# Kernel optimization log

Hardware: AMD Instinct MI355X
Metric: run time of the kernel (lower is better)

Reference implementation:

```python
import jax, jax.numpy as jnp
import numpy as np

N_NODES = 50000
N_EDGES = 800000
D_IN = 128
D_OUT = 128
ALPHA = 0.5


def setup_inputs() -> dict:
    key = jax.random.key(0)
    k1, k2, k3, k4, k5, k6 = jax.random.split(key, 6)
    x = jax.random.normal(k1, (N_NODES, D_IN), dtype=jnp.float32)
    edge_index = jax.random.randint(k2, (2, N_EDGES), 0, N_NODES, dtype=jnp.int32)
    s = 1.0 / np.sqrt(D_IN)  # torch.nn.Linear default init bound
    W_src = jax.random.uniform(k3, (D_IN, D_OUT), jnp.float32, -s, s)
    b_src = jax.random.uniform(k4, (D_OUT,), jnp.float32, -s, s)
    W_dst = jax.random.uniform(k5, (D_IN, D_OUT), jnp.float32, -s, s)
    b_dst = jax.random.uniform(k6, (D_OUT,), jnp.float32, -s, s)
    return {"x": x, "edge_index": edge_index, "W_src": W_src, "b_src": b_src,
            "W_dst": W_dst, "b_dst": b_dst}


def reference(x, edge_index, W_src, b_src, W_dst, b_dst):
    row, col = edge_index[0], edge_index[1]
    ones = jnp.ones((row.shape[0],), dtype=x.dtype)
    # out-degree = row sums of A; in-degree = column sums of A
    out_deg = jax.ops.segment_sum(ones, row, num_segments=N_NODES)
    in_deg = jax.ops.segment_sum(ones, col, num_segments=N_NODES)
    d_out = jnp.where(out_deg > 0, out_deg ** -0.5, 0.0)
    d_in = jnp.where(in_deg > 0, in_deg ** -0.5, 0.0)
    # D_out^{-1/2} A D_in^{-1/2}: per-edge weight. For A^T the normalized
    # weight at (col,row) is d_in[col]*d_out[row] == same weight, transposed scatter.
    w = d_out[row] * d_in[col]  # [E]
    msg_fwd = w[:, None] * x[col]  # [E, D_IN]
    agg_fwd = jax.ops.segment_sum(msg_fwd, row, num_segments=N_NODES)  # adj_norm @ x
    msg_bwd = w[:, None] * x[row]
    agg_bwd = jax.ops.segment_sum(msg_bwd, col, num_segments=N_NODES)  # adj_t_norm @ x
    out = ALPHA * (agg_fwd @ W_src + b_src) + (1.0 - ALPHA) * (agg_bwd @ W_dst + b_dst)
    return out
```

## Files before the change

kernel.cpp:

```cpp
#include <hip/hip_runtime.h>
#include <hip/hip_bf16.h>


constexpr int N_NODES = 50000;
constexpr int N_EDGES = 800000;
constexpr int D = 128;
constexpr int CAP = 48;
constexpr int NPBK = 512;
constexpr int NBUK = (N_NODES + NPBK - 1) / NPBK;
constexpr int ECH = 2048;
constexpr int NCH = (N_EDGES + ECH - 1) / ECH;
constexpr int CAPB = 12288;
constexpr int CVTB = 128;

typedef __bf16 bf16x8 __attribute__((ext_vector_type(8)));
typedef float  f32x4  __attribute__((ext_vector_type(4)));

__global__ __launch_bounds__(256) void k_part(const int* __restrict__ row,
                                              const int* __restrict__ col,
                                              int* __restrict__ tail,
                                              unsigned* __restrict__ part,
                                              const float* __restrict__ Wsrc,
                                              const float* __restrict__ Wdst,
                                              __hip_bfloat16* __restrict__ Wpk,
                                              const float* __restrict__ x,
                                              __hip_bfloat16* __restrict__ xb) {
    const int bid = blockIdx.x;
    if (bid >= NCH * 2 + 16) {
        const float4* x4 = (const float4*)x;
        bf16x8* xb8 = (bf16x8*)xb;
        const int stride = CVTB * 256;
        for (int i = (bid - (NCH * 2 + 16)) * 256 + threadIdx.x;
             i < N_NODES * D / 8; i += stride) {
            float4 v0 = x4[2 * i];
            float4 v1 = x4[2 * i + 1];
            union { bf16x8 v; __hip_bfloat16 e[8]; } u;
            u.e[0] = __float2bfloat16(v0.x); u.e[1] = __float2bfloat16(v0.y);
            u.e[2] = __float2bfloat16(v0.z); u.e[3] = __float2bfloat16(v0.w);
            u.e[4] = __float2bfloat16(v1.x); u.e[5] = __float2bfloat16(v1.y);
            u.e[6] = __float2bfloat16(v1.z); u.e[7] = __float2bfloat16(v1.w);
            xb8[i] = u.v;
        }
        return;
    }
    if (bid >= NCH * 2) {
        int tid = (bid - NCH * 2) * 256 + threadIdx.x;
        int f = tid >> 6;
        int lane = tid & 63;
        int dir = f >> 5;
        int ct = (f >> 2) & 7;
        int ks = f & 3;
        const float* W = dir ? Wdst : Wsrc;
        int k0 = ks * 32 + (lane >> 4) * 8;
        int n = ct * 16 + (lane & 15);
        __hip_bfloat16 v[8];
        #pragma unroll
        for (int j = 0; j < 8; ++j) v[j] = __float2bfloat16(W[(k0 + j) * D + n]);
        *(bf16x8*)&Wpk[(size_t)tid * 8] = *(const bf16x8*)v;
        return;
    }
    __shared__ int cnt[NBUK], base[NBUK], pos[NBUK];
    const int dir = bid & 1;
    const int chunk = bid >> 1;
    const int* dst = dir ? col : row;
    const int* src = dir ? row : col;
    for (int i = threadIdx.x; i < NBUK; i += 256) { cnt[i] = 0; pos[i] = 0; }
    __syncthreads();
    const int e0 = chunk * ECH;
    const int e1 = min(e0 + ECH, N_EDGES);
    for (int e = e0 + threadIdx.x; e < e1; e += 256)
        atomicAdd(&cnt[dst[e] >> 9], 1);
    __syncthreads();
    for (int i = threadIdx.x; i < NBUK; i += 256)
        base[i] = (cnt[i] > 0) ? atomicAdd(&tail[dir * NBUK + i], cnt[i]) : 0;
    __syncthreads();
    for (int e = e0 + threadIdx.x; e < e1; e += 256) {
        int d = dst[e], s = src[e];
        int b = d >> 9;
        int p = base[b] + atomicAdd(&pos[b], 1);
        if (p < CAPB)
            part[((size_t)dir * NBUK + b) * CAPB + p] =
                ((unsigned)(d & (NPBK - 1)) << 16) | (unsigned)s;
    }
}

__global__ __launch_bounds__(256) void k_bin(const int* __restrict__ tail,
                                             const unsigned* __restrict__ part,
                                             unsigned short* __restrict__ binF,
                                             unsigned short* __restrict__ binB,
                                             int* __restrict__ cntF,
                                             int* __restrict__ cntB,
                                             float* __restrict__ sc_row,
                                             float* __restrict__ sc_col) {
    __shared__ alignas(16) unsigned short bins[NPBK * CAP];
    __shared__ int cnt[NPBK];
    const int dir = blockIdx.x & 1;
    const int b = blockIdx.x >> 1;
    for (int i = threadIdx.x; i < NPBK; i += 256) cnt[i] = 0;
    __syncthreads();
    const int n = min(tail[dir * NBUK + b], CAPB);
    const unsigned* p = &part[((size_t)dir * NBUK + b) * CAPB];
    for (int i = threadIdx.x; i < n; i += 256) {
        unsigned ent = p[i];
        int dl = ent >> 16;
        int q = atomicAdd(&cnt[dl], 1);
        if (q < CAP) bins[dl * CAP + q] = (unsigned short)(ent & 0xFFFFu);
    }
    __syncthreads();
    unsigned short* gbin = dir ? binB : binF;
    int* gcnt = dir ? cntB : cntF;
    float* sc = dir ? sc_col : sc_row;
    const int node0 = b * NPBK;
    const int nv = min(NPBK, N_NODES - node0);
    const int nq = nv * (CAP * 2 / 16);
    const uint4* bw = (const uint4*)bins;
    uint4* gw = (uint4*)&gbin[(size_t)node0 * CAP];
    for (int i = threadIdx.x; i < nq; i += 256) gw[i] = bw[i];
    for (int i = threadIdx.x; i < nv; i += 256) {
        int c = cnt[i];
        gcnt[node0 + i] = c;
        sc[node0 + i] = (c > 0) ? rsqrtf((float)c) : 0.f;
    }
}

__device__ __forceinline__ float4 bf4_to_f4(uint2 u) {
    union { unsigned i; float f; } a, b, c, d;
    a.i = u.x << 16;
    b.i = u.x & 0xFFFF0000u;
    c.i = u.y << 16;
    d.i = u.y & 0xFFFF0000u;
    return make_float4(a.f, b.f, c.f, d.f);
}

__device__ __forceinline__ uint2 f4_to_bf4(float4 f) {
    union { uint2 u; __hip_bfloat16 e[4]; } r;
    r.e[0] = __float2bfloat16(f.x);
    r.e[1] = __float2bfloat16(f.y);
    r.e[2] = __float2bfloat16(f.z);
    r.e[3] = __float2bfloat16(f.w);
    return r.u;
}

__global__ __launch_bounds__(256) void k_agg(const unsigned short* __restrict__ binF,
                                             const int* __restrict__ cntF,
                                             const unsigned short* __restrict__ binB,
                                             const int* __restrict__ cntB,
                                             const float* __restrict__ sc_row,
                                             const float* __restrict__ sc_col,
                                             const uint2* __restrict__ xb,
                                             __hip_bfloat16* __restrict__ aggF,
                                             __hip_bfloat16* __restrict__ aggB) {
    const int node = blockIdx.x * 4 + (threadIdx.x >> 6);
    const int lane = threadIdx.x & 63;
    const int half = lane >> 5;
    const int l32 = lane & 31;
    const int nF = min(cntF[node], CAP);
    const int nB = min(cntB[node], CAP);

    int entF = (lane < nF) ? (int)binF[(size_t)node * CAP + lane] : 0;
    int entB = (lane < nB) ? (int)binB[(size_t)node * CAP + lane] : 0;
    float sclF = sc_col[entF];
    float sclB = sc_row[entB];

    const int sTailF = __shfl(entF, (nF > 0) ? nF - 1 : 0);
    const int sTailB = __shfl(entB, (nB > 0) ? nB - 1 : 0);
    const float wTailF = __shfl(sclF, (nF > 0) ? nF - 1 : 0);
    const float wTailB = __shfl(sclB, (nB > 0) ? nB - 1 : 0);

    float4 accF = make_float4(0.f, 0.f, 0.f, 0.f);
    {
        const int npair = nF >> 1;
        int i = 0;
        for (; i + 3 < npair; i += 4) {
            int s0 = __shfl(entF, 2 * i + half);
            int s1 = __shfl(entF, 2 * (i + 1) + half);
            int s2 = __shfl(entF, 2 * (i + 2) + half);
            int s3 = __shfl(entF, 2 * (i + 3) + half);
            float w0 = __shfl(sclF, 2 * i + half);
            float w1 = __shfl(sclF, 2 * (i + 1) + half);
            float w2 = __shfl(sclF, 2 * (i + 2) + half);
            float w3 = __shfl(sclF, 2 * (i + 3) + half);
            uint2 v0 = xb[(size_t)s0 * 32 + l32];
            uint2 v1 = xb[(size_t)s1 * 32 + l32];
            uint2 v2 = xb[(size_t)s2 * 32 + l32];
            uint2 v3 = xb[(size_t)s3 * 32 + l32];
            float4 f0 = bf4_to_f4(v0), f1 = bf4_to_f4(v1);
            float4 f2 = bf4_to_f4(v2), f3 = bf4_to_f4(v3);
            accF.x += w0 * f0.x + w1 * f1.x + w2 * f2.x + w3 * f3.x;
            accF.y += w0 * f0.y + w1 * f1.y + w2 * f2.y + w3 * f3.y;
            accF.z += w0 * f0.z + w1 * f1.z + w2 * f2.z + w3 * f3.z;
            accF.w += w0 * f0.w + w1 * f1.w + w2 * f2.w + w3 * f3.w;
        }
        for (; i < npair; ++i) {
            int s = __shfl(entF, 2 * i + half);
            float w = __shfl(sclF, 2 * i + half);
            float4 f = bf4_to_f4(xb[(size_t)s * 32 + l32]);
            accF.x += w * f.x; accF.y += w * f.y;
            accF.z += w * f.z; accF.w += w * f.w;
        }
        if ((nF & 1) && half == 0) {
            float4 f = bf4_to_f4(xb[(size_t)sTailF * 32 + l32]);
            accF.x += wTailF * f.x; accF.y += wTailF * f.y;
            accF.z += wTailF * f.z; accF.w += wTailF * f.w;
        }
    }
    float4 accB = make_float4(0.f, 0.f, 0.f, 0.f);
    {
        const int npair = nB >> 1;
        int i = 0;
        for (; i + 3 < npair; i += 4) {
            int s0 = __shfl(entB, 2 * i + half);
            int s1 = __shfl(entB, 2 * (i + 1) + half);
            int s2 = __shfl(entB, 2 * (i + 2) + half);
            int s3 = __shfl(entB, 2 * (i + 3) + half);
            float w0 = __shfl(sclB, 2 * i + half);
            float w1 = __shfl(sclB, 2 * (i + 1) + half);
            float w2 = __shfl(sclB, 2 * (i + 2) + half);
            float w3 = __shfl(sclB, 2 * (i + 3) + half);
            uint2 v0 = xb[(size_t)s0 * 32 + l32];
            uint2 v1 = xb[(size_t)s1 * 32 + l32];
            uint2 v2 = xb[(size_t)s2 * 32 + l32];
            uint2 v3 = xb[(size_t)s3 * 32 + l32];
            float4 f0 = bf4_to_f4(v0), f1 = bf4_to_f4(v1);
            float4 f2 = bf4_to_f4(v2), f3 = bf4_to_f4(v3);
            accB.x += w0 * f0.x + w1 * f1.x + w2 * f2.x + w3 * f3.x;
            accB.y += w0 * f0.y + w1 * f1.y + w2 * f2.y + w3 * f3.y;
            accB.z += w0 * f0.z + w1 * f1.z + w2 * f2.z + w3 * f3.z;
            accB.w += w0 * f0.w + w1 * f1.w + w2 * f2.w + w3 * f3.w;
        }
        for (; i < npair; ++i) {
            int s = __shfl(entB, 2 * i + half);
            float w = __shfl(sclB, 2 * i + half);
            float4 f = bf4_to_f4(xb[(size_t)s * 32 + l32]);
            accB.x += w * f.x; accB.y += w * f.y;
            accB.z += w * f.z; accB.w += w * f.w;
        }
        if ((nB & 1) && half == 0) {
            float4 f = bf4_to_f4(xb[(size_t)sTailB * 32 + l32]);
            accB.x += wTailB * f.x; accB.y += wTailB * f.y;
            accB.z += wTailB * f.z; accB.w += wTailB * f.w;
        }
    }

    accF.x += __shfl_xor(accF.x, 32);
    accF.y += __shfl_xor(accF.y, 32);
    accF.z += __shfl_xor(accF.z, 32);
    accF.w += __shfl_xor(accF.w, 32);
    accB.x += __shfl_xor(accB.x, 32);
    accB.y += __shfl_xor(accB.y, 32);
    accB.z += __shfl_xor(accB.z, 32);
    accB.w += __shfl_xor(accB.w, 32);

    if (half == 0) {
        float s = 0.5f * sc_row[node];
        ((uint2*)aggF)[(size_t)node * 32 + l32] =
            f4_to_bf4(make_float4(s * accF.x, s * accF.y, s * accF.z, s * accF.w));
    } else {
        float s = 0.5f * sc_col[node];
        ((uint2*)aggB)[(size_t)node * 32 + l32] =
            f4_to_bf4(make_float4(s * accB.x, s * accB.y, s * accB.z, s * accB.w));
    }
}

__global__ __launch_bounds__(256) void k_gemm_out(const __hip_bfloat16* __restrict__ aggF,
                                                  const __hip_bfloat16* __restrict__ aggB,
                                                  const bf16x8* __restrict__ Wpk,
                                                  const float* __restrict__ b_src,
                                                  const float* __restrict__ b_dst,
                                                  float* __restrict__ out) {
    __shared__ bf16x8 Bs[64 * 64];
    for (int i = threadIdx.x; i < 64 * 64; i += 256) Bs[i] = Wpk[i];

    const int wave = threadIdx.x >> 6;
    const int lane = threadIdx.x & 63;
    const int quad = lane >> 4;
    const int m0 = blockIdx.x * 64 + wave * 16;

    const int arow = min(m0 + (lane & 15), N_NODES - 1);
    bf16x8 aF[4], aB[4];
    #pragma unroll
    for (int ks = 0; ks < 4; ++ks) {
        aF[ks] = *(const bf16x8*)&aggF[(size_t)arow * D + ks * 32 + quad * 8];
        aB[ks] = *(const bf16x8*)&aggB[(size_t)arow * D + ks * 32 + quad * 8];
    }

    __syncthreads();

    const int crow = m0 + quad * 4;
    #pragma unroll
    for (int ct = 0; ct < 8; ++ct) {
        f32x4 c = {0.f, 0.f, 0.f, 0.f};
        #pragma unroll
        for (int ks = 0; ks < 4; ++ks)
            c = __builtin_amdgcn_mfma_f32_16x16x32_bf16(aF[ks], Bs[(ct * 4 + ks) * 64 + lane], c, 0, 0, 0);
        #pragma unroll
        for (int ks = 0; ks < 4; ++ks)
            c = __builtin_amdgcn_mfma_f32_16x16x32_bf16(aB[ks], Bs[(32 + ct * 4 + ks) * 64 + lane], c, 0, 0, 0);
        const int colb = ct * 16 + (lane & 15);
        const float bias = 0.5f * (b_src[colb] + b_dst[colb]);
        #pragma unroll
        for (int r = 0; r < 4; ++r) {
            int nd = crow + r;
            if (nd < N_NODES) out[(size_t)nd * D + colb] = c[r] + bias;
        }
    }
}

extern "C" void kernel_launch(void* const* d_in, const int* in_sizes, int n_in,
                              void* d_out, int out_size, void* d_ws, size_t ws_size,
                              hipStream_t stream) {
    const float* x     = (const float*)d_in[0];
    const int*   edges = (const int*)d_in[1];
    const float* W_src = (const float*)d_in[2];
    const float* b_src = (const float*)d_in[3];
    const float* W_dst = (const float*)d_in[4];
    const float* b_dst = (const float*)d_in[5];
    float* out = (float*)d_out;

    const int* row = edges;
    const int* col = edges + N_EDGES;

    __hip_bfloat16* xb     = (__hip_bfloat16*)d_ws;
    __hip_bfloat16* aggF   = xb + (size_t)N_NODES * D;
    __hip_bfloat16* aggB   = aggF + (size_t)N_NODES * D;
    __hip_bfloat16* Wpk    = aggB + (size_t)N_NODES * D;
    float*          sc_row = (float*)(Wpk + 64 * 512);
    float*          sc_col = sc_row + N_NODES;
    int*            cntF   = (int*)(sc_col + N_NODES);
    int*            cntB   = cntF + N_NODES;
    int*            tail   = cntB + N_NODES;
    unsigned short* binF   = (unsigned short*)(tail + 256);
    unsigned short* binB   = binF + (size_t)N_NODES * CAP;
    unsigned*       part   = (unsigned*)aggF;

    (void)hipMemsetAsync(tail, 0, 256 * sizeof(int), stream);

    const int gP = NCH * 2 + 16 + CVTB;
    const int gB = NBUK * 2;
    const int gA = N_NODES / 4;
    const int gM = (N_NODES + 63) / 64;

    k_part<<<gP, 256, 0, stream>>>(row, col, tail, part, W_src, W_dst, Wpk, x, xb);
    k_bin<<<gB, 256, 0, stream>>>(tail, part, binF, binB, cntF, cntB, sc_row, sc_col);
    k_agg<<<gA, 256, 0, stream>>>(binF, cntF, binB, cntB, sc_row, sc_col,
                                  (const uint2*)xb, aggF, aggB);
    k_gemm_out<<<gM, 256, 0, stream>>>(aggF, aggB, (const bf16x8*)Wpk,
                                       b_src, b_dst, out);
}
```

Baseline: 198.4 us.

## Tile aggregation gather by source-node range for cache locality

Rewrites the aggregation kernel so each wave owns a strided set of destination nodes in one direction and sweeps source-id tiles, only gathering edges whose source falls in the current tile. This aims to keep the gathered feature rows resident in cache during each tile pass. In exchange, every tile pass reloads bins and counts, adds ballot/ctz serialization with at most two gathers in flight, and loads per-edge scales individually, reducing memory-level parallelism.

```diff
diff --git a/kernel.cpp b/kernel.cpp
--- a/kernel.cpp
+++ b/kernel.cpp
@@ -12,6 +12,12 @@
 constexpr int NCH = (N_EDGES + ECH - 1) / ECH;
 constexpr int CAPB = 12288;
 constexpr int CVTB = 128;
+
+constexpr int TSH  = 13;
+constexpr int NT   = (N_NODES + (1 << TSH) - 1) >> TSH;
+constexpr int AGGB = 1024;
+constexpr int DWID = AGGB * 4 / 2;
+constexpr int KMAX = (N_NODES + DWID - 1) / DWID;
 
 typedef __bf16 bf16x8 __attribute__((ext_vector_type(8)));
 typedef float  f32x4  __attribute__((ext_vector_type(4)));
@@ -123,142 +129,74 @@
     }
 }
 
-__device__ __forceinline__ float4 bf4_to_f4(uint2 u) {
-    union { unsigned i; float f; } a, b, c, d;
-    a.i = u.x << 16;
-    b.i = u.x & 0xFFFF0000u;
-    c.i = u.y << 16;
-    d.i = u.y & 0xFFFF0000u;
-    return make_float4(a.f, b.f, c.f, d.f);
-}
-
-__device__ __forceinline__ uint2 f4_to_bf4(float4 f) {
-    union { uint2 u; __hip_bfloat16 e[4]; } r;
-    r.e[0] = __float2bfloat16(f.x);
-    r.e[1] = __float2bfloat16(f.y);
-    r.e[2] = __float2bfloat16(f.z);
-    r.e[3] = __float2bfloat16(f.w);
-    return r.u;
-}
-
-__global__ __launch_bounds__(256) void k_agg(const unsigned short* __restrict__ binF,
-                                             const int* __restrict__ cntF,
-                                             const unsigned short* __restrict__ binB,
-                                             const int* __restrict__ cntB,
-                                             const float* __restrict__ sc_row,
-                                             const float* __restrict__ sc_col,
-                                             const uint2* __restrict__ xb,
-                                             __hip_bfloat16* __restrict__ aggF,
-                                             __hip_bfloat16* __restrict__ aggB) {
-    const int node = blockIdx.x * 4 + (threadIdx.x >> 6);
+__global__ __launch_bounds__(256, 4) void k_agg(const unsigned short* __restrict__ binF,
+                                                const int* __restrict__ cntF,
+                                                const unsigned short* __restrict__ binB,
+                                                const int* __restrict__ cntB,
+                                                const float* __restrict__ sc_row,
+                                                const float* __restrict__ sc_col,
+                                                const unsigned* __restrict__ xb32,
+                                                unsigned* __restrict__ aggF32,
+                                                unsigned* __restrict__ aggB32) {
+    const int wid  = blockIdx.x * 4 + (threadIdx.x >> 6);
     const int lane = threadIdx.x & 63;
-    const int half = lane >> 5;
-    const int l32 = lane & 31;
-    const int nF = min(cntF[node], CAP);
-    const int nB = min(cntB[node], CAP);
-
-    int entF = (lane < nF) ? (int)binF[(size_t)node * CAP + lane] : 0;
-    int entB = (lane < nB) ? (int)binB[(size_t)node * CAP + lane] : 0;
-    float sclF = sc_col[entF];
-    float sclB = sc_row[entB];
-
-    const int sTailF = __shfl(entF, (nF > 0) ? nF - 1 : 0);
-    const int sTailB = __shfl(entB, (nB > 0) ? nB - 1 : 0);
-    const float wTailF = __shfl(sclF, (nF > 0) ? nF - 1 : 0);
-    const float wTailB = __shfl(sclB, (nB > 0) ? nB - 1 : 0);
-
-    float4 accF = make_float4(0.f, 0.f, 0.f, 0.f);
-    {
-        const int npair = nF >> 1;
-        int i = 0;
-        for (; i + 3 < npair; i += 4) {
-            int s0 = __shfl(entF, 2 * i + half);
-            int s1 = __shfl(entF, 2 * (i + 1) + half);
-            int s2 = __shfl(entF, 2 * (i + 2) + half);
-            int s3 = __shfl(entF, 2 * (i + 3) + half);
-            float w0 = __shfl(sclF, 2 * i + half);
-            float w1 = __shfl(sclF, 2 * (i + 1) + half);
-            float w2 = __shfl(sclF, 2 * (i + 2) + half);
-            float w3 = __shfl(sclF, 2 * (i + 3) + half);
-            uint2 v0 = xb[(size_t)s0 * 32 + l32];
-            uint2 v1 = xb[(size_t)s1 * 32 + l32];
-            uint2 v2 = xb[(size_t)s2 * 32 + l32];
-            uint2 v3 = xb[(size_t)s3 * 32 + l32];
-            float4 f0 = bf4_to_f4(v0), f1 = bf4_to_f4(v1);
-            float4 f2 = bf4_to_f4(v2), f3 = bf4_to_f4(v3);
-            accF.x += w0 * f0.x + w1 * f1.x + w2 * f2.x + w3 * f3.x;
-            accF.y += w0 * f0.y + w1 * f1.y + w2 * f2.y + w3 * f3.y;
-            accF.z += w0 * f0.z + w1 * f1.z + w2 * f2.z + w3 * f3.z;
-            accF.w += w0 * f0.w + w1 * f1.w + w2 * f2.w + w3 * f3.w;
-        }
-        for (; i < npair; ++i) {
-            int s = __shfl(entF, 2 * i + half);
-            float w = __shfl(sclF, 2 * i + half);
-            float4 f = bf4_to_f4(xb[(size_t)s * 32 + l32]);
-            accF.x += w * f.x; accF.y += w * f.y;
-            accF.z += w * f.z; accF.w += w * f.w;
-        }
-        if ((nF & 1) && half == 0) {
-            float4 f = bf4_to_f4(xb[(size_t)sTailF * 32 + l32]);
-            accF.x += wTailF * f.x; accF.y += wTailF * f.y;
-            accF.z += wTailF * f.z; accF.w += wTailF * f.w;
-        }
-    }
-    float4 accB = make_float4(0.f, 0.f, 0.f, 0.f);
-    {
-        const int npair = nB >> 1;
-        int i = 0;
-        for (; i + 3 < npair; i += 4) {
-            int s0 = __shfl(entB, 2 * i + half);
-            int s1 = __shfl(entB, 2 * (i + 1) + half);
-            int s2 = __shfl(entB, 2 * (i + 2) + half);
-            int s3 = __shfl(entB, 2 * (i + 3) + half);
-            float w0 = __shfl(sclB, 2 * i + half);
-            float w1 = __shfl(sclB, 2 * (i + 1) + half);
-            float w2 = __shfl(sclB, 2 * (i + 2) + half);
-            float w3 = __shfl(sclB, 2 * (i + 3) + half);
-            uint2 v0 = xb[(size_t)s0 * 32 + l32];
-            uint2 v1 = xb[(size_t)s1 * 32 + l32];
-            uint2 v2 = xb[(size_t)s2 * 32 + l32];
-            uint2 v3 = xb[(size_t)s3 * 32 + l32];
-            float4 f0 = bf4_to_f4(v0), f1 = bf4_to_f4(v1);
-            float4 f2 = bf4_to_f4(v2), f3 = bf4_to_f4(v3);
-            accB.x += w0 * f0.x + w1 * f1.x + w2 * f2.x + w3 * f3.x;
-            accB.y += w0 * f0.y + w1 * f1.y + w2 * f2.y + w3 * f3.y;
-            accB.z += w0 * f0.z + w1 * f1.z + w2 * f2.z + w3 * f3.z;
-            accB.w += w0 * f0.w + w1 * f1.w + w2 * f2.w + w3 * f3.w;
-        }
-        for (; i < npair; ++i) {
-            int s = __shfl(entB, 2 * i + half);
-            float w = __shfl(sclB, 2 * i + half);
-            float4 f = bf4_to_f4(xb[(size_t)s * 32 + l32]);
-            accB.x += w * f.x; accB.y += w * f.y;
-            accB.z += w * f.z; accB.w += w * f.w;
-        }
-        if ((nB & 1) && half == 0) {
-            float4 f = bf4_to_f4(xb[(size_t)sTailB * 32 + l32]);
-            accB.x += wTailB * f.x; accB.y += wTailB * f.y;
-            accB.z += wTailB * f.z; accB.w += wTailB * f.w;
-        }
-    }
-
-    accF.x += __shfl_xor(accF.x, 32);
-    accF.y += __shfl_xor(accF.y, 32);
-    accF.z += __shfl_xor(accF.z, 32);
-    accF.w += __shfl_xor(accF.w, 32);
-    accB.x += __shfl_xor(accB.x, 32);
-    accB.y += __shfl_xor(accB.y, 32);
-    accB.z += __shfl_xor(accB.z, 32);
-    accB.w += __shfl_xor(accB.w, 32);
-
-    if (half == 0) {
-        float s = 0.5f * sc_row[node];
-        ((uint2*)aggF)[(size_t)node * 32 + l32] =
-            f4_to_bf4(make_float4(s * accF.x, s * accF.y, s * accF.z, s * accF.w));
-    } else {
-        float s = 0.5f * sc_col[node];
-        ((uint2*)aggB)[(size_t)node * 32 + l32] =
-            f4_to_bf4(make_float4(s * accB.x, s * accB.y, s * accB.z, s * accB.w));
+    const int dir  = wid & 1;
+    const int dwid = wid >> 1;
+
+    const unsigned short* bin = dir ? binB : binF;
+    const int*   cnt  = dir ? cntB : cntF;
+    const float* sc_s = dir ? sc_row : sc_col;
+    const float* sc_d = dir ? sc_col : sc_row;
+    unsigned*    agg  = dir ? aggB32 : aggF32;
+
+    float2 acc[KMAX];
+    #pragma unroll
+    for (int k = 0; k < KMAX; ++k) acc[k] = make_float2(0.f, 0.f);
+
+    for (int t = 0; t < NT; ++t) {
+        #pragma unroll
+        for (int k = 0; k < KMAX; ++k) {
+            const int node = dwid + k * DWID;
+            if (node < N_NODES) {
+                const int n = min(cnt[node], CAP);
+                int ent = (int)bin[(size_t)node * CAP + min(lane, CAP - 1)];
+                ent = (lane < n) ? ent : 0xFFFF;
+                unsigned long long m = __ballot((ent >> TSH) == t);
+                while (m) {
+                    int i0 = __builtin_ctzll(m); m &= m - 1;
+                    int s0 = __shfl(ent, i0);
+                    unsigned v0 = xb32[(size_t)s0 * 64 + lane];
+                    float w0 = sc_s[s0];
+                    int have1 = (m != 0);
+                    int s1 = 0; unsigned v1 = 0; float w1 = 0.f;
+                    if (have1) {
+                        int i1 = __builtin_ctzll(m); m &= m - 1;
+                        s1 = __shfl(ent, i1);
+                        v1 = xb32[(size_t)s1 * 64 + lane];
+                        w1 = sc_s[s1];
+                    }
+                    union { unsigned u; float f; } a, b;
+                    a.u = v0 << 16; b.u = v0 & 0xFFFF0000u;
+                    acc[k].x += w0 * a.f; acc[k].y += w0 * b.f;
+                    if (have1) {
+                        a.u = v1 << 16; b.u = v1 & 0xFFFF0000u;
+                        acc[k].x += w1 * a.f; acc[k].y += w1 * b.f;
+                    }
+                }
+            }
+        }
+    }
+
+    #pragma unroll
+    for (int k = 0; k < KMAX; ++k) {
+        const int node = dwid + k * DWID;
+        if (node < N_NODES) {
+            float s = 0.5f * sc_d[node];
+            union { unsigned u; __hip_bfloat16 e[2]; } r;
+            r.e[0] = __float2bfloat16(s * acc[k].x);
+            r.e[1] = __float2bfloat16(s * acc[k].y);
+            agg[(size_t)node * 64 + lane] = r.u;
+        }
     }
 }
 
@@ -337,13 +275,12 @@
 
     const int gP = NCH * 2 + 16 + CVTB;
     const int gB = NBUK * 2;
-    const int gA = N_NODES / 4;
     const int gM = (N_NODES + 63) / 64;
 
     k_part<<<gP, 256, 0, stream>>>(row, col, tail, part, W_src, W_dst, Wpk, x, xb);
     k_bin<<<gB, 256, 0, stream>>>(tail, part, binF, binB, cntF, cntB, sc_row, sc_col);
-    k_agg<<<gA, 256, 0, stream>>>(binF, cntF, binB, cntB, sc_row, sc_col,
-                                  (const uint2*)xb, aggF, aggB);
+    k_agg<<<AGGB, 256, 0, stream>>>(binF, cntF, binB, cntB, sc_row, sc_col,
+                                    (const unsigned*)xb, (unsigned*)aggF, (unsigned*)aggB);
     k_gemm_out<<<gM, 256, 0, stream>>>(aggF, aggB, (const bf16x8*)Wpk,
                                        b_src, b_dst, out);
 }
```

Result: slower. 364.2 us (+83.6%).

## Fuse all stages into one persistent cooperative kernel with grid syncs

Applied to the files above, without the earlier changes.

Replaces the memset plus four separate kernel launches with a single cooperative persistent kernel. The stages are convert/pack, partition, bin, aggregate and GEMM, separated by grid.sync and run in grid-stride task loops. Bucket size is halved to 256 nodes so the binning shared memory fits alongside higher occupancy. The GEMM now reads packed weights straight from global memory instead of staging them in LDS. The aim is to remove launch gaps and tail effects between stages, at the cost of grid-wide barriers and fewer blocks resident per stage.

```diff
diff --git a/kernel.cpp b/kernel.cpp
--- a/kernel.cpp
+++ b/kernel.cpp
@@ -1,37 +1,68 @@
 #include <hip/hip_runtime.h>
 #include <hip/hip_bf16.h>
+#include <hip/hip_cooperative_groups.h>
+
+namespace cg = cooperative_groups;
 
 
 constexpr int N_NODES = 50000;
 constexpr int N_EDGES = 800000;
 constexpr int D = 128;
 constexpr int CAP = 48;
-constexpr int NPBK = 512;
+constexpr int NPBK = 256;
 constexpr int NBUK = (N_NODES + NPBK - 1) / NPBK;
 constexpr int ECH = 2048;
 constexpr int NCH = (N_EDGES + ECH - 1) / ECH;
-constexpr int CAPB = 12288;
-constexpr int CVTB = 128;
+constexpr int CAPB = 5120;
 
 typedef __bf16 bf16x8 __attribute__((ext_vector_type(8)));
 typedef float  f32x4  __attribute__((ext_vector_type(4)));
 
-__global__ __launch_bounds__(256) void k_part(const int* __restrict__ row,
-                                              const int* __restrict__ col,
-                                              int* __restrict__ tail,
-                                              unsigned* __restrict__ part,
-                                              const float* __restrict__ Wsrc,
-                                              const float* __restrict__ Wdst,
-                                              __hip_bfloat16* __restrict__ Wpk,
-                                              const float* __restrict__ x,
-                                              __hip_bfloat16* __restrict__ xb) {
-    const int bid = blockIdx.x;
-    if (bid >= NCH * 2 + 16) {
-        const float4* x4 = (const float4*)x;
-        bf16x8* xb8 = (bf16x8*)xb;
-        const int stride = CVTB * 256;
-        for (int i = (bid - (NCH * 2 + 16)) * 256 + threadIdx.x;
-             i < N_NODES * D / 8; i += stride) {
+struct Params {
+    const int* row; const int* col;
+    const float* x; const float* Wsrc; const float* Wdst;
+    const float* bsrc; const float* bdst;
+    __hip_bfloat16* xb;
+    __hip_bfloat16* Wpk;
+    int* tail; unsigned* part;
+    unsigned short* binF; unsigned short* binB;
+    int* cntF; int* cntB;
+    float* sc_row; float* sc_col;
+    __hip_bfloat16* aggF; __hip_bfloat16* aggB;
+    float* out;
+};
+
+__global__ __launch_bounds__(256, 4) void k_all(Params P) {
+    cg::grid_group grid = cg::this_grid();
+    const int bid  = blockIdx.x;
+    const int nblk = gridDim.x;
+    const int tid  = threadIdx.x;
+    const int wave = tid >> 6;
+    const int lane = tid & 63;
+
+    __shared__ union {
+        struct { int cnt[NBUK]; int base[NBUK]; int pos[NBUK]; } p1;
+        struct { alignas(16) unsigned short bins[NPBK * CAP]; int cnt[NPBK]; } p2;
+    } sh;
+
+    if (bid == 0)
+        for (int i = tid; i < 2 * NBUK; i += 256) P.tail[i] = 0;
+    if (bid >= 1 && bid <= 16) {
+        int t = (bid - 1) * 256 + tid;
+        int f = t >> 6, l = t & 63;
+        int dir = f >> 5, ct = (f >> 2) & 7, ks = f & 3;
+        const float* W = dir ? P.Wdst : P.Wsrc;
+        int k0 = ks * 32 + (l >> 4) * 8;
+        int n = ct * 16 + (l & 15);
+        __hip_bfloat16 v[8];
+        #pragma unroll
+        for (int j = 0; j < 8; ++j) v[j] = __float2bfloat16(W[(k0 + j) * D + n]);
+        *(bf16x8*)&P.Wpk[(size_t)t * 8] = *(const bf16x8*)v;
+    }
+    {
+        const float4* x4 = (const float4*)P.x;
+        bf16x8* xb8 = (bf16x8*)P.xb;
+        for (int i = bid * 256 + tid; i < N_NODES * D / 8; i += nblk * 256) {
             float4 v0 = x4[2 * i];
             float4 v1 = x4[2 * i + 1];
             union { bf16x8 v; __hip_bfloat16 e[8]; } u;
@@ -41,267 +72,255 @@
             u.e[6] = __float2bfloat16(v1.z); u.e[7] = __float2bfloat16(v1.w);
             xb8[i] = u.v;
         }
-        return;
-    }
-    if (bid >= NCH * 2) {
-        int tid = (bid - NCH * 2) * 256 + threadIdx.x;
-        int f = tid >> 6;
-        int lane = tid & 63;
-        int dir = f >> 5;
-        int ct = (f >> 2) & 7;
-        int ks = f & 3;
-        const float* W = dir ? Wdst : Wsrc;
-        int k0 = ks * 32 + (lane >> 4) * 8;
-        int n = ct * 16 + (lane & 15);
-        __hip_bfloat16 v[8];
-        #pragma unroll
-        for (int j = 0; j < 8; ++j) v[j] = __float2bfloat16(W[(k0 + j) * D + n]);
-        *(bf16x8*)&Wpk[(size_t)tid * 8] = *(const bf16x8*)v;
-        return;
-    }
-    __shared__ int cnt[NBUK], base[NBUK], pos[NBUK];
-    const int dir = bid & 1;
-    const int chunk = bid >> 1;
-    const int* dst = dir ? col : row;
-    const int* src = dir ? row : col;
-    for (int i = threadIdx.x; i < NBUK; i += 256) { cnt[i] = 0; pos[i] = 0; }
-    __syncthreads();
-    const int e0 = chunk * ECH;
-    const int e1 = min(e0 + ECH, N_EDGES);
-    for (int e = e0 + threadIdx.x; e < e1; e += 256)
-        atomicAdd(&cnt[dst[e] >> 9], 1);
-    __syncthreads();
-    for (int i = threadIdx.x; i < NBUK; i += 256)
-        base[i] = (cnt[i] > 0) ? atomicAdd(&tail[dir * NBUK + i], cnt[i]) : 0;
-    __syncthreads();
-    for (int e = e0 + threadIdx.x; e < e1; e += 256) {
-        int d = dst[e], s = src[e];
-        int b = d >> 9;
-        int p = base[b] + atomicAdd(&pos[b], 1);
-        if (p < CAPB)
-            part[((size_t)dir * NBUK + b) * CAPB + p] =
-                ((unsigned)(d & (NPBK - 1)) << 16) | (unsigned)s;
-    }
-}
-
-__global__ __launch_bounds__(256) void k_bin(const int* __restrict__ tail,
-                                             const unsigned* __restrict__ part,
-                                             unsigned short* __restrict__ binF,
-                                             unsigned short* __restrict__ binB,
-                                             int* __restrict__ cntF,
-                                             int* __restrict__ cntB,
-                                             float* __restrict__ sc_row,
-                                             float* __restrict__ sc_col) {
-    __shared__ alignas(16) unsigned short bins[NPBK * CAP];
-    __shared__ int cnt[NPBK];
-    const int dir = blockIdx.x & 1;
-    const int b = blockIdx.x >> 1;
-    for (int i = threadIdx.x; i < NPBK; i += 256) cnt[i] = 0;
-    __syncthreads();
-    const int n = min(tail[dir * NBUK + b], CAPB);
-    const unsigned* p = &part[((size_t)dir * NBUK + b) * CAPB];
-    for (int i = threadIdx.x; i < n; i += 256) {
-        unsigned ent = p[i];
-        int dl = ent >> 16;
-        int q = atomicAdd(&cnt[dl], 1);
-        if (q < CAP) bins[dl * CAP + q] = (unsigned short)(ent & 0xFFFFu);
-    }
-    __syncthreads();
-    unsigned short* gbin = dir ? binB : binF;
-    int* gcnt = dir ? cntB : cntF;
-    float* sc = dir ? sc_col : sc_row;
-    const int node0 = b * NPBK;
-    const int nv = min(NPBK, N_NODES - node0);
-    const int nq = nv * (CAP * 2 / 16);
-    const uint4* bw = (const uint4*)bins;
-    uint4* gw = (uint4*)&gbin[(size_t)node0 * CAP];
-    for (int i = threadIdx.x; i < nq; i += 256) gw[i] = bw[i];
-    for (int i = threadIdx.x; i < nv; i += 256) {
-        int c = cnt[i];
-        gcnt[node0 + i] = c;
-        sc[node0 + i] = (c > 0) ? rsqrtf((float)c) : 0.f;
-    }
-}
-
-__device__ __forceinline__ float4 bf4_to_f4(uint2 u) {
-    union { unsigned i; float f; } a, b, c, d;
-    a.i = u.x << 16;
-    b.i = u.x & 0xFFFF0000u;
-    c.i = u.y << 16;
-    d.i = u.y & 0xFFFF0000u;
-    return make_float4(a.f, b.f, c.f, d.f);
-}
-
-__device__ __forceinline__ uint2 f4_to_bf4(float4 f) {
-    union { uint2 u; __hip_bfloat16 e[4]; } r;
-    r.e[0] = __float2bfloat16(f.x);
-    r.e[1] = __float2bfloat16(f.y);
-    r.e[2] = __float2bfloat16(f.z);
-    r.e[3] = __float2bfloat16(f.w);
-    return r.u;
-}
-
-__global__ __launch_bounds__(256) void k_agg(const unsigned short* __restrict__ binF,
-                                             const int* __restrict__ cntF,
-                                             const unsigned short* __restrict__ binB,
-                                             const int* __restrict__ cntB,
-                                             const float* __restrict__ sc_row,
-                                             const float* __restrict__ sc_col,
-                                             const uint2* __restrict__ xb,
-                                             __hip_bfloat16* __restrict__ aggF,
-                                             __hip_bfloat16* __restrict__ aggB) {
-    const int node = blockIdx.x * 4 + (threadIdx.x >> 6);
-    const int lane = threadIdx.x & 63;
-    const int half = lane >> 5;
-    const int l32 = lane & 31;
-    const int nF = min(cntF[node], CAP);
-    const int nB = min(cntB[node], CAP);
-
-    int entF = (lane < nF) ? (int)binF[(size_t)node * CAP + lane] : 0;
-    int entB = (lane < nB) ? (int)binB[(size_t)node * CAP + lane] : 0;
-    float sclF = sc_col[entF];
-    float sclB = sc_row[entB];
-
-    const int sTailF = __shfl(entF, (nF > 0) ? nF - 1 : 0);
-    const int sTailB = __shfl(entB, (nB > 0) ? nB - 1 : 0);
-    const float wTailF = __shfl(sclF, (nF > 0) ? nF - 1 : 0);
-    const float wTailB = __shfl(sclB, (nB > 0) ? nB - 1 : 0);
-
-    float4 accF = make_float4(0.f, 0.f, 0.f, 0.f);
+    }
+    grid.sync();
+
+    for (int task = bid; task < NCH * 2; task += nblk) {
+        const int dir = task & 1, chunk = task >> 1;
+        const int* dst = dir ? P.col : P.row;
+        const int* src = dir ? P.row : P.col;
+        for (int i = tid; i < NBUK; i += 256) { sh.p1.cnt[i] = 0; sh.p1.pos[i] = 0; }
+        __syncthreads();
+        const int e0 = chunk * ECH;
+        const int e1 = min(e0 + ECH, N_EDGES);
+        for (int e = e0 + tid; e < e1; e += 256)
+            atomicAdd(&sh.p1.cnt[dst[e] >> 8], 1);
+        __syncthreads();
+        for (int i = tid; i < NBUK; i += 256)
+            sh.p1.base[i] = (sh.p1.cnt[i] > 0)
+                          ? atomicAdd(&P.tail[dir * NBUK + i], sh.p1.cnt[i]) : 0;
+        __syncthreads();
+        for (int e = e0 + tid; e < e1; e += 256) {
+            int d = dst[e], s = src[e];
+            int b = d >> 8;
+            int p = sh.p1.base[b] + atomicAdd(&sh.p1.pos[b], 1);
+            if (p < CAPB)
+                P.part[((size_t)dir * NBUK + b) * CAPB + p] =
+                    ((unsigned)(d & (NPBK - 1)) << 16) | (unsigned)s;
+        }
+        __syncthreads();
+    }
+    grid.sync();
+
+    for (int task = bid; task < NBUK * 2; task += nblk) {
+        const int dir = task & 1, bk = task >> 1;
+        for (int i = tid; i < NPBK; i += 256) sh.p2.cnt[i] = 0;
+        __syncthreads();
+        const int n = min(P.tail[dir * NBUK + bk], CAPB);
+        const unsigned* p = &P.part[((size_t)dir * NBUK + bk) * CAPB];
+        for (int i = tid; i < n; i += 256) {
+            unsigned ent = p[i];
+            int dl = ent >> 16;
+            int q = atomicAdd(&sh.p2.cnt[dl], 1);
+            if (q < CAP) sh.p2.bins[dl * CAP + q] = (unsigned short)(ent & 0xFFFFu);
+        }
+        __syncthreads();
+        unsigned short* gbin = dir ? P.binB : P.binF;
+        int* gcnt = dir ? P.cntB : P.cntF;
+        float* sc = dir ? P.sc_col : P.sc_row;
+        const int node0 = bk * NPBK;
+        const int nv = min(NPBK, N_NODES - node0);
+        const int nq = nv * (CAP * 2 / 16);
+        const uint4* bw = (const uint4*)sh.p2.bins;
+        uint4* gw = (uint4*)&gbin[(size_t)node0 * CAP];
+        for (int i = tid; i < nq; i += 256) gw[i] = bw[i];
+        for (int i = tid; i < nv; i += 256) {
+            int c = sh.p2.cnt[i];
+            gcnt[node0 + i] = c;
+            sc[node0 + i] = (c > 0) ? rsqrtf((float)c) : 0.f;
+        }
+        __syncthreads();
+    }
+    grid.sync();
+
     {
-        const int npair = nF >> 1;
-        int i = 0;
-        for (; i + 3 < npair; i += 4) {
-            int s0 = __shfl(entF, 2 * i + half);
-            int s1 = __shfl(entF, 2 * (i + 1) + half);
-            int s2 = __shfl(entF, 2 * (i + 2) + half);
-            int s3 = __shfl(entF, 2 * (i + 3) + half);
-            float w0 = __shfl(sclF, 2 * i + half);
-            float w1 = __shfl(sclF, 2 * (i + 1) + half);
-            float w2 = __shfl(sclF, 2 * (i + 2) + half);
-            float w3 = __shfl(sclF, 2 * (i + 3) + half);
-            uint2 v0 = xb[(size_t)s0 * 32 + l32];
-            uint2 v1 = xb[(size_t)s1 * 32 + l32];
-            uint2 v2 = xb[(size_t)s2 * 32 + l32];
-            uint2 v3 = xb[(size_t)s3 * 32 + l32];
-            float4 f0 = bf4_to_f4(v0), f1 = bf4_to_f4(v1);
-            float4 f2 = bf4_to_f4(v2), f3 = bf4_to_f4(v3);
-            accF.x += w0 * f0.x + w1 * f1.x + w2 * f2.x + w3 * f3.x;
-            accF.y += w0 * f0.y + w1 * f1.y + w2 * f2.y + w3 * f3.y;
-            accF.z += w0 * f0.z + w1 * f1.z + w2 * f2.z + w3 * f3.z;
-            accF.w += w0 * f0.w + w1 * f1.w + w2 * f2.w + w3 * f3.w;
-        }
-        for (; i < npair; ++i) {
-            int s = __shfl(entF, 2 * i + half);
-            float w = __shfl(sclF, 2 * i + half);
-            float4 f = bf4_to_f4(xb[(size_t)s * 32 + l32]);
-            accF.x += w * f.x; accF.y += w * f.y;
-            accF.z += w * f.z; accF.w += w * f.w;
-        }
-        if ((nF & 1) && half == 0) {
-            float4 f = bf4_to_f4(xb[(size_t)sTailF * 32 + l32]);
-            accF.x += wTailF * f.x; accF.y += wTailF * f.y;
-            accF.z += wTailF * f.z; accF.w += wTailF * f.w;
-        }
-    }
-    float4 accB = make_float4(0.f, 0.f, 0.f, 0.f);
+        const int half = lane >> 5;
+        const int l32 = lane & 31;
+        const uint2* xb2 = (const uint2*)P.xb;
+        for (int nb = bid; nb < N_NODES / 4; nb += nblk) {
+            const int node = nb * 4 + wave;
+            const int nF = min(P.cntF[node], CAP);
+            const int nB = min(P.cntB[node], CAP);
+
+            int entF = (lane < nF) ? (int)P.binF[(size_t)node * CAP + lane] : 0;
+            int entB = (lane < nB) ? (int)P.binB[(size_t)node * CAP + lane] : 0;
+            float sclF = P.sc_col[entF];
+            float sclB = P.sc_row[entB];
+
+            const int sTailF = __shfl(entF, (nF > 0) ? nF - 1 : 0);
+            const int sTailB = __shfl(entB, (nB > 0) ? nB - 1 : 0);
+            const float wTailF = __shfl(sclF, (nF > 0) ? nF - 1 : 0);
+            const float wTailB = __shfl(sclB, (nB > 0) ? nB - 1 : 0);
+
+            float4 accF = make_float4(0.f, 0.f, 0.f, 0.f);
+            {
+                const int npair = nF >> 1;
+                int i = 0;
+                for (; i + 3 < npair; i += 4) {
+                    int s0 = __shfl(entF, 2 * i + half);
+                    int s1 = __shfl(entF, 2 * (i + 1) + half);
+                    int s2 = __shfl(entF, 2 * (i + 2) + half);
+                    int s3 = __shfl(entF, 2 * (i + 3) + half);
+                    float w0 = __shfl(sclF, 2 * i + half);
+                    float w1 = __shfl(sclF, 2 * (i + 1) + half);
+                    float w2 = __shfl(sclF, 2 * (i + 2) + half);
+                    float w3 = __shfl(sclF, 2 * (i + 3) + half);
+                    uint2 v0 = xb2[(size_t)s0 * 32 + l32];
+                    uint2 v1 = xb2[(size_t)s1 * 32 + l32];
+                    uint2 v2 = xb2[(size_t)s2 * 32 + l32];
+                    uint2 v3 = xb2[(size_t)s3 * 32 + l32];
+                    union { unsigned u; float f; } a, b;
+                    a.u = v0.x << 16; b.u = v0.x & 0xFFFF0000u;
+                    accF.x += w0 * a.f; accF.y += w0 * b.f;
+                    a.u = v0.y << 16; b.u = v0.y & 0xFFFF0000u;
+                    accF.z += w0 * a.f; accF.w += w0 * b.f;
+                    a.u = v1.x << 16; b.u = v1.x & 0xFFFF0000u;
+                    accF.x += w1 * a.f; accF.y += w1 * b.f;
+                    a.u = v1.y << 16; b.u = v1.y & 0xFFFF0000u;
+                    accF.z += w1 * a.f; accF.w += w1 * b.f;
+                    a.u = v2.x << 16; b.u = v2.x & 0xFFFF0000u;
+                    accF.x += w2 * a.f; accF.y += w2 * b.f;
+                    a.u = v2.y << 16; b.u = v2.y & 0xFFFF0000u;
+                    accF.z += w2 * a.f; accF.w += w2 * b.f;
+                    a.u = v3.x << 16; b.u = v3.x & 0xFFFF0000u;
+                    accF.x += w3 * a.f; accF.y += w3 * b.f;
+                    a.u = v3.y << 16; b.u = v3.y & 0xFFFF0000u;
+                    accF.z += w3 * a.f; accF.w += w3 * b.f;
+                }
+                for (; i < npair; ++i) {
+                    int s = __shfl(entF, 2 * i + half);
+                    float w = __shfl(sclF, 2 * i + half);
+                    uint2 v = xb2[(size_t)s * 32 + l32];
+                    union { unsigned u; float f; } a, b;
+                    a.u = v.x << 16; b.u = v.x & 0xFFFF0000u;
+                    accF.x += w * a.f; accF.y += w * b.f;
+                    a.u = v.y << 16; b.u = v.y & 0xFFFF0000u;
+                    accF.z += w * a.f; accF.w += w * b.f;
+                }
+                if ((nF & 1) && half == 0) {
+                    uint2 v = xb2[(size_t)sTailF * 32 + l32];
+                    union { unsigned u; float f; } a, b;
+                    a.u = v.x << 16; b.u = v.x & 0xFFFF0000u;
+                    accF.x += wTailF * a.f; accF.y += wTailF * b.f;
+                    a.u = v.y << 16; b.u = v.y & 0xFFFF0000u;
+                    accF.z += wTailF * a.f; accF.w += wTailF * b.f;
+                }
+            }
+            float4 accB = make_float4(0.f, 0.f, 0.f, 0.f);
+            {
+                const int npair = nB >> 1;
+                int i = 0;
+                for (; i + 3 < npair; i += 4) {
+                    int s0 = __shfl(entB, 2 * i + half);
+                    int s1 = __shfl(entB, 2 * (i + 1) + half);
+                    int s2 = __shfl(entB, 2 * (i + 2) + half);
+                    int s3 = __shfl(entB, 2 * (i + 3) + half);
+                    float w0 = __shfl(sclB, 2 * i + half);
+                    float w1 = __shfl(sclB, 2 * (i + 1) + half);
+                    float w2 = __shfl(sclB, 2 * (i + 2) + half);
+                    float w3 = __shfl(sclB, 2 * (i + 3) + half);
+                    uint2 v0 = xb2[(size_t)s0 * 32 + l32];
+                    uint2 v1 = xb2[(size_t)s1 * 32 + l32];
+                    uint2 v2 = xb2[(size_t)s2 * 32 + l32];
+                    uint2 v3 = xb2[(size_t)s3 * 32 + l32];
+                    union { unsigned u; float f; } a, b;
+                    a.u = v0.x << 16; b.u = v0.x & 0xFFFF0000u;
+                    accB.x += w0 * a.f; accB.y += w0 * b.f;
+                    a.u = v0.y << 16; b.u = v0.y & 0xFFFF0000u;
+                    accB.z += w0 * a.f; accB.w += w0 * b.f;
+                    a.u = v1.x << 16; b.u = v1.x & 0xFFFF0000u;
+                    accB.x += w1 * a.f; accB.y += w1 * b.f;
+                    a.u = v1.y << 16; b.u = v1.y & 0xFFFF0000u;
+                    accB.z += w1 * a.f; accB.w += w1 * b.f;
+                    a.u = v2.x << 16; b.u = v2.x & 0xFFFF0000u;
+                    accB.x += w2 * a.f; accB.y += w2 * b.f;
+                    a.u = v2.y << 16; b.u = v2.y & 0xFFFF0000u;
+                    accB.z += w2 * a.f; accB.w += w2 * b.f;
+                    a.u = v3.x << 16; b.u = v3.x & 0xFFFF0000u;
+                    accB.x += w3 * a.f; accB.y += w3 * b.f;
+                    a.u = v3.y << 16; b.u = v3.y & 0xFFFF0000u;
+                    accB.z += w3 * a.f; accB.w += w3 * b.f;
+                }
+                for (; i < npair; ++i) {
+                    int s = __shfl(entB, 2 * i + half);
+                    float w = __shfl(sclB, 2 * i + half);
+                    uint2 v = xb2[(size_t)s * 32 + l32];
+                    union { unsigned u; float f; } a, b;
+                    a.u = v.x << 16; b.u = v.x & 0xFFFF0000u;
+                    accB.x += w * a.f; accB.y += w * b.f;
+                    a.u = v.y << 16; b.u = v.y & 0xFFFF0000u;
+                    accB.z += w * a.f; accB.w += w * b.f;
+                }
+                if ((nB & 1) && half == 0) {
+                    uint2 v = xb2[(size_t)sTailB * 32 + l32];
+                    union { unsigned u; float f; } a, b;
+                    a.u = v.x << 16; b.u = v.x & 0xFFFF0000u;
+                    accB.x += wTailB * a.f; accB.y += wTailB * b.f;
+                    a.u = v.y << 16; b.u = v.y & 0xFFFF0000u;
+                    accB.z += wTailB * a.f; accB.w += wTailB * b.f;
+                }
+            }
+
+            accF.x += __shfl_xor(accF.x, 32);
+            accF.y += __shfl_xor(accF.y, 32);
+            accF.z += __shfl_xor(accF.z, 32);
+            accF.w += __shfl_xor(accF.w, 32);
+            accB.x += __shfl_xor(accB.x, 32);
+            accB.y += __shfl_xor(accB.y, 32);
+            accB.z += __shfl_xor(accB.z, 32);
+            accB.w += __shfl_xor(accB.w, 32);
+
+            if (half == 0) {
+                float s = 0.5f * P.sc_row[node];
+                union { uint2 u; __hip_bfloat16 e[4]; } r;
+                r.e[0] = __float2bfloat16(s * accF.x);
+                r.e[1] = __float2bfloat16(s * accF.y);
+                r.e[2] = __float2bfloat16(s * accF.z);
+                r.e[3] = __float2bfloat16(s * accF.w);
+                ((uint2*)P.aggF)[(size_t)node * 32 + l32] = r.u;
+            } else {
+                float s = 0.5f * P.sc_col[node];
+                union { uint2 u; __hip_bfloat16 e[4]; } r;
+                r.e[0] = __float2bfloat16(s * accB.x);
+                r.e[1] = __float2bfloat16(s * accB.y);
+                r.e[2] = __float2bfloat16(s * accB.z);
+                r.e[3] = __float2bfloat16(s * accB.w);
+                ((uint2*)P.aggB)[(size_t)node * 32 + l32] = r.u;
+            }
+        }
+    }
+    grid.sync();
+
     {
-        const int npair = nB >> 1;
-        int i = 0;
-        for (; i + 3 < npair; i += 4) {
-            int s0 = __shfl(entB, 2 * i + half);
-            int s1 = __shfl(entB, 2 * (i + 1) + half);
-            int s2 = __shfl(entB, 2 * (i + 2) + half);
-            int s3 = __shfl(entB, 2 * (i + 3) + half);
-            float w0 = __shfl(sclB, 2 * i + half);
-            float w1 = __shfl(sclB, 2 * (i + 1) + half);
-            float w2 = __shfl(sclB, 2 * (i + 2) + half);
-            float w3 = __shfl(sclB, 2 * (i + 3) + half);
-            uint2 v0 = xb[(size_t)s0 * 32 + l32];
-            uint2 v1 = xb[(size_t)s1 * 32 + l32];
-            uint2 v2 = xb[(size_t)s2 * 32 + l32];
-            uint2 v3 = xb[(size_t)s3 * 32 + l32];
-            float4 f0 = bf4_to_f4(v0), f1 = bf4_to_f4(v1);
-            float4 f2 = bf4_to_f4(v2), f3 = bf4_to_f4(v3);
-            accB.x += w0 * f0.x + w1 * f1.x + w2 * f2.x + w3 * f3.x;
-            accB.y += w0 * f0.y + w1 * f1.y + w2 * f2.y + w3 * f3.y;
-            accB.z += w0 * f0.z + w1 * f1.z + w2 * f2.z + w3 * f3.z;
-            accB.w += w0 * f0.w + w1 * f1.w + w2 * f2.w + w3 * f3.w;
-        }
-        for (; i < npair; ++i) {
-            int s = __shfl(entB, 2 * i + half);
-            float w = __shfl(sclB, 2 * i + half);
-            float4 f = bf4_to_f4(xb[(size_t)s * 32 + l32]);
-            accB.x += w * f.x; accB.y += w * f.y;
-            accB.z += w * f.z; accB.w += w * f.w;
-        }
-        if ((nB & 1) && half == 0) {
-            float4 f = bf4_to_f4(xb[(size_t)sTailB * 32 + l32]);
-            accB.x += wTailB * f.x; accB.y += wTailB * f.y;
-            accB.z += wTailB * f.z; accB.w += wTailB * f.w;
-        }
-    }
-
-    accF.x += __shfl_xor(accF.x, 32);
-    accF.y += __shfl_xor(accF.y, 32);
-    accF.z += __shfl_xor(accF.z, 32);
-    accF.w += __shfl_xor(accF.w, 32);
-    accB.x += __shfl_xor(accB.x, 32);
-    accB.y += __shfl_xor(accB.y, 32);
-    accB.z += __shfl_xor(accB.z, 32);
-    accB.w += __shfl_xor(accB.w, 32);
-
-    if (half == 0) {
-        float s = 0.5f * sc_row[node];
-        ((uint2*)aggF)[(size_t)node * 32 + l32] =
-            f4_to_bf4(make_float4(s * accF.x, s * accF.y, s * accF.z, s * accF.w));
-    } else {
-        float s = 0.5f * sc_col[node];
-        ((uint2*)aggB)[(size_t)node * 32 + l32] =
-            f4_to_bf4(make_float4(s * accB.x, s * accB.y, s * accB.z, s * accB.w));
-    }
-}
-
-__global__ __launch_bounds__(256) void k_gemm_out(const __hip_bfloat16* __restrict__ aggF,
-                                                  const __hip_bfloat16* __restrict__ aggB,
-                                                  const bf16x8* __restrict__ Wpk,
-                                                  const float* __restrict__ b_src,
-                                                  const float* __restrict__ b_dst,
-                                                  float* __restrict__ out) {
-    __shared__ bf16x8 Bs[64 * 64];
-    for (int i = threadIdx.x; i < 64 * 64; i += 256) Bs[i] = Wpk[i];
-
-    const int wave = threadIdx.x >> 6;
-    const int lane = threadIdx.x & 63;
-    const int quad = lane >> 4;
-    const int m0 = blockIdx.x * 64 + wave * 16;
-
-    const int arow = min(m0 + (lane & 15), N_NODES - 1);
-    bf16x8 aF[4], aB[4];
-    #pragma unroll
-    for (int ks = 0; ks < 4; ++ks) {
-        aF[ks] = *(const bf16x8*)&aggF[(size_t)arow * D + ks * 32 + quad * 8];
-        aB[ks] = *(const bf16x8*)&aggB[(size_t)arow * D + ks * 32 + quad * 8];
-    }
-
-    __syncthreads();
-
-    const int crow = m0 + quad * 4;
-    #pragma unroll
-    for (int ct = 0; ct < 8; ++ct) {
-        f32x4 c = {0.f, 0.f, 0.f, 0.f};
-        #pragma unroll
-        for (int ks = 0; ks < 4; ++ks)
-            c = __builtin_amdgcn_mfma_f32_16x16x32_bf16(aF[ks], Bs[(ct * 4 + ks) * 64 + lane], c, 0, 0, 0);
-        #pragma unroll
-        for (int ks = 0; ks < 4; ++ks)
-            c = __builtin_amdgcn_mfma_f32_16x16x32_bf16(aB[ks], Bs[(32 + ct * 4 + ks) * 64 + lane], c, 0, 0, 0);
-        const int colb = ct * 16 + (lane & 15);
-        const float bias = 0.5f * (b_src[colb] + b_dst[colb]);
-        #pragma unroll
-        for (int r = 0; r < 4; ++r) {
-            int nd = crow + r;
-            if (nd < N_NODES) out[(size_t)nd * D + colb] = c[r] + bias;
+        const int quad = lane >> 4;
+        const bf16x8* Wg = (const bf16x8*)P.Wpk;
+        for (int tile = bid; tile < (N_NODES + 63) / 64; tile += nblk) {
+            const int m0 = tile * 64 + wave * 16;
+            const int arow = min(m0 + (lane & 15), N_NODES - 1);
+            bf16x8 aF[4], aB[4];
+            #pragma unroll
+            for (int ks = 0; ks < 4; ++ks) {
+                aF[ks] = *(const bf16x8*)&P.aggF[(size_t)arow * D + ks * 32 + quad * 8];
+                aB[ks] = *(const bf16x8*)&P.aggB[(size_t)arow * D + ks * 32 + quad * 8];
+            }
+            const int crow = m0 + quad * 4;
+            #pragma unroll
+            for (int ct = 0; ct < 8; ++ct) {
+                f32x4 c = {0.f, 0.f, 0.f, 0.f};
+                #pragma unroll
+                for (int ks = 0; ks < 4; ++ks)
+                    c = __builtin_amdgcn_mfma_f32_16x16x32_bf16(aF[ks], Wg[(ct * 4 + ks) * 64 + lane], c, 0, 0, 0);
+                #pragma unroll
+                for (int ks = 0; ks < 4; ++ks)
+                    c = __builtin_amdgcn_mfma_f32_16x16x32_bf16(aB[ks], Wg[2048 + (ct * 4 + ks) * 64 + lane], c, 0, 0, 0);
+                const int colb = ct * 16 + (lane & 15);
+                const float bias = 0.5f * (P.bsrc[colb] + P.bdst[colb]);
+                #pragma unroll
+                for (int r = 0; r < 4; ++r) {
+                    int nd = crow + r;
+                    if (nd < N_NODES) P.out[(size_t)nd * D + colb] = c[r] + bias;
+                }
+            }
         }
     }
 }
@@ -315,10 +334,6 @@
     const float* b_src = (const float*)d_in[3];
     const float* W_dst = (const float*)d_in[4];
     const float* b_dst = (const float*)d_in[5];
-    float* out = (float*)d_out;
-
-    const int* row = edges;
-    const int* col = edges + N_EDGES;
 
     __hip_bfloat16* xb     = (__hip_bfloat16*)d_ws;
     __hip_bfloat16* aggF   = xb + (size_t)N_NODES * D;
@@ -329,21 +344,30 @@
     int*            cntF   = (int*)(sc_col + N_NODES);
     int*            cntB   = cntF + N_NODES;
     int*            tail   = cntB + N_NODES;
-    unsigned short* binF   = (unsigned short*)(tail + 256);
+    unsigned short* binF   = (unsigned short*)(tail + 512);
     unsigned short* binB   = binF + (size_t)N_NODES * CAP;
     unsigned*       part   = (unsigned*)aggF;
 
-    (void)hipMemsetAsync(tail, 0, 256 * sizeof(int), stream);
-
-    const int gP = NCH * 2 + 16 + CVTB;
-    const int gB = NBUK * 2;
-    const int gA = N_NODES / 4;
-    const int gM = (N_NODES + 63) / 64;
-
-    k_part<<<gP, 256, 0, stream>>>(row, col, tail, part, W_src, W_dst, Wpk, x, xb);
-    k_bin<<<gB, 256, 0, stream>>>(tail, part, binF, binB, cntF, cntB, sc_row, sc_col);
-    k_agg<<<gA, 256, 0, stream>>>(binF, cntF, binB, cntB, sc_row, sc_col,
-                                  (const uint2*)xb, aggF, aggB);
-    k_gemm_out<<<gM, 256, 0, stream>>>(aggF, aggB, (const bf16x8*)Wpk,
-                                       b_src, b_dst, out);
+    Params P;
+    P.row = edges; P.col = edges + N_EDGES;
+    P.x = x; P.Wsrc = W_src; P.Wdst = W_dst; P.bsrc = b_src; P.bdst = b_dst;
+    P.xb = xb; P.Wpk = Wpk;
+    P.tail = tail; P.part = part;
+    P.binF = binF; P.binB = binB; P.cntF = cntF; P.cntB = cntB;
+    P.sc_row = sc_row; P.sc_col = sc_col;
+    P.aggF = aggF; P.aggB = aggB;
+    P.out = (float*)d_out;
+
+    static int nblk = 0;
+    if (nblk == 0) {
+        int bpc = 0;
+        hipError_t e = hipOccupancyMaxActiveBlocksPerMultiprocessor(&bpc, k_all, 256, 0);
+        if (e != hipSuccess || bpc < 1) bpc = 2;
+        nblk = bpc * 256;
+        if (nblk > 2048) nblk = 2048;
+    }
+
+    void* args[] = { (void*)&P };
+    (void)hipLaunchCooperativeKernel((const void*)k_all, dim3(nblk), dim3(256),
+                                     args, 0, stream);
 }
```

New measurement: 544.8 us. 175% more time.
